# Optimization experiments

Hardware: AMD Instinct MI355X
Metric: run time of the kernel (lower is better)

The kernel has to match this reference:

```python
import jax, jax.numpy as jnp
import numpy as np

B, L, D, H, MLP = 8, 1024, 768, 12, 3072
DH = D // H
EPS = 1e-5


def setup_inputs() -> dict:
    key = jax.random.key(0)
    ks = jax.random.split(key, 8)
    s = 0.02
    return {
        "x": jax.random.normal(ks[0], (B, L, D), dtype=jnp.float32),
        "ln1_g": jnp.ones((D,), jnp.float32),
        "ln1_b": jnp.zeros((D,), jnp.float32),
        "w_qkv": jax.random.normal(ks[1], (3 * D, D), dtype=jnp.float32) * s,
        "w_out": jax.random.normal(ks[2], (D, D), dtype=jnp.float32) * s,
        "b_out": jnp.zeros((D,), jnp.float32),
        "ln2_g": jnp.ones((D,), jnp.float32),
        "ln2_b": jnp.zeros((D,), jnp.float32),
        "w1": jax.random.normal(ks[3], (MLP, D), dtype=jnp.float32) * s,
        "b1": jnp.zeros((MLP,), jnp.float32),
        "w2": jax.random.normal(ks[4], (D, MLP), dtype=jnp.float32) * s,
        "b2": jnp.zeros((D,), jnp.float32),
    }


def _layernorm(x, g, b):
    mu = jnp.mean(x, axis=-1, keepdims=True)
    var = jnp.mean(jnp.square(x - mu), axis=-1, keepdims=True)
    return (x - mu) * jax.lax.rsqrt(var + EPS) * g + b


def reference(x, ln1_g, ln1_b, w_qkv, w_out, b_out, ln2_g, ln2_b, w1, b1, w2, b2):
    # --- self-attention branch ---
    xn = _layernorm(x, ln1_g, ln1_b)                     # [B, L, D]
    qkv = jnp.einsum('bld,ed->ble', xn, w_qkv)           # [B, L, 3D]
    # rearrange 'b l (qkv h d) -> qkv b h l d'
    qkv = qkv.reshape(B, L, 3, H, DH).transpose(2, 0, 3, 1, 4)
    q, k, v = qkv[0], qkv[1], qkv[2]                     # [B, H, L, DH]
    scale = DH ** -0.5
    att = jnp.einsum('bhxd,bhyd->bhxy', q, k) * scale    # [B, H, L, L]
    att = jax.nn.softmax(att, axis=-1)
    o = jnp.einsum('bhxy,bhyd->bhxd', att, v)            # [B, H, L, DH]
    o = o.transpose(0, 2, 1, 3).reshape(B, L, D)         # 'b h l d -> b l (h d)'
    o = jnp.einsum('bld,ed->ble', o, w_out) + b_out
    x = x + o
    # --- MLP branch ---
    xn = _layernorm(x, ln2_g, ln2_b)
    h = jax.nn.gelu(jnp.einsum('bld,md->blm', xn, w1) + b1, approximate=False)
    h = jnp.einsum('blm,dm->bld', h, w2) + b2
    return x + h
```

## Files before the change

kernel.cpp:

```cpp
#include <hip/hip_runtime.h>
#include <hip/hip_bf16.h>
#include <math.h>

#define NB 8
#define NL 1024
#define ND 768
#define NH 12
#define NDH 64
#define NMLP 3072
#define NROWS 8192

typedef __attribute__((ext_vector_type(8))) short short8;
typedef __attribute__((ext_vector_type(8))) __bf16 bf16x8;
typedef __attribute__((ext_vector_type(4))) float f32x4;
typedef __attribute__((ext_vector_type(4))) float float4v;
typedef __attribute__((ext_vector_type(4))) unsigned short ushort4v;

__device__ __forceinline__ unsigned short f2b(float f) {
  unsigned u = __float_as_uint(f);
  unsigned r = (u + 0x7fffu + ((u >> 16) & 1u)) >> 16;
  return (unsigned short)r;
}

__device__ __forceinline__ f32x4 mfma16(short8 a, short8 b, f32x4 c) {
  return __builtin_amdgcn_mfma_f32_16x16x32_bf16(
      __builtin_bit_cast(bf16x8, a), __builtin_bit_cast(bf16x8, b), c, 0, 0, 0);
}

__device__ __forceinline__ void gl_lds16(const void* g, void* l) {
  __builtin_amdgcn_global_load_lds(
      (__attribute__((address_space(1))) void*)g,
      (__attribute__((address_space(3))) void*)l, 16, 0, 0);
}

__global__ __launch_bounds__(256) void cvt_bf16(const float* __restrict__ s,
                                                unsigned short* __restrict__ d,
                                                int n) {
  int i = (blockIdx.x * 256 + threadIdx.x) * 4;
  if (i < n) {
    float4v v = *(const float4v*)(s + i);
    ushort4v o;
    o[0] = f2b(v[0]); o[1] = f2b(v[1]); o[2] = f2b(v[2]); o[3] = f2b(v[3]);
    *(ushort4v*)(d + i) = o;
  }
}

__global__ __launch_bounds__(256) void ln_bf16(const float* __restrict__ x,
                                               const float* __restrict__ g,
                                               const float* __restrict__ b,
                                               unsigned short* __restrict__ out) {
  int row = blockIdx.x, tid = threadIdx.x;
  const float* xr = x + (size_t)row * ND;
  float v0 = xr[tid], v1 = xr[tid + 256], v2 = xr[tid + 512];
  float s = v0 + v1 + v2;
  __shared__ float red[8];
#pragma unroll
  for (int o = 32; o > 0; o >>= 1) s += __shfl_down(s, o);
  int wv = tid >> 6, ln = tid & 63;
  if (ln == 0) red[wv] = s;
  __syncthreads();
  float mu = (red[0] + red[1] + red[2] + red[3]) * (1.0f / 768.0f);
  float d0 = v0 - mu, d1 = v1 - mu, d2 = v2 - mu;
  float q = d0 * d0 + d1 * d1 + d2 * d2;
#pragma unroll
  for (int o = 32; o > 0; o >>= 1) q += __shfl_down(q, o);
  if (ln == 0) red[4 + wv] = q;
  __syncthreads();
  float var = (red[4] + red[5] + red[6] + red[7]) * (1.0f / 768.0f);
  float rs = rsqrtf(var + 1e-5f);
  unsigned short* orow = out + (size_t)row * ND;
  orow[tid]       = f2b(d0 * rs * g[tid]       + b[tid]);
  orow[tid + 256] = f2b(d1 * rs * g[tid + 256] + b[tid + 256]);
  orow[tid + 512] = f2b(d2 * rs * g[tid + 512] + b[tid + 512]);
}

template <int MODE, int BM>
__global__ __launch_bounds__(256) void gemm_bt(
    const unsigned short* __restrict__ A, const unsigned short* __restrict__ W,
    unsigned short* __restrict__ outB, float* __restrict__ outF,
    const float* __restrict__ bias, const float* __restrict__ resid,
    int M, int N, int K, int gx) {
  constexpr int WN = (BM == 128) ? 2 : 4;
  constexpr int NJ = 128 / (WN * 16);
  __shared__ __attribute__((aligned(16))) unsigned short As[2 * BM * 32];
  __shared__ __attribute__((aligned(16))) unsigned short Bs[2 * 128 * 32];

  const int nwg = gridDim.x;
  const int bid = blockIdx.x;
  const int q = nwg >> 3, r = nwg & 7;
  const int xcd = bid & 7, idx = bid >> 3;
  const int swz = (xcd < r ? xcd * (q + 1) : r * (q + 1) + (xcd - r) * q) + idx;
  const int by = swz / gx, bx = swz - by * gx;
  const int m0 = by * BM, n0 = bx * 128;

  const int tid = threadIdx.x;
  const int wave = tid >> 6, lane = tid & 63;
  const int l15 = lane & 15, lhi = lane >> 4;
  const int wm = wave / WN, wn = wave % WN;

  const int sr = tid >> 2, sc8 = (tid & 3) * 8;
  const unsigned short* Ag0 = A + (size_t)(m0 + sr) * K + sc8;
  const unsigned short* Ag1 = Ag0 + (size_t)64 * K;
  const unsigned short* Wg0 = W + (size_t)(n0 + sr) * K + sc8;
  const unsigned short* Wg1 = Wg0 + (size_t)64 * K;

  f32x4 acc[4][NJ];
#pragma unroll
  for (int i = 0; i < 4; i++)
#pragma unroll
    for (int j = 0; j < NJ; j++) acc[i][j] = (f32x4){0.f, 0.f, 0.f, 0.f};

  auto STAGE = [&](int k0v, int buf) {
    unsigned short* Ad = As + buf * (BM * 32) + wave * 512;
    unsigned short* Bd = Bs + buf * 4096 + wave * 512;
    gl_lds16(Ag0 + k0v, Ad);
    if constexpr (BM == 128) gl_lds16(Ag1 + k0v, Ad + 2048);
    gl_lds16(Wg0 + k0v, Bd);
    gl_lds16(Wg1 + k0v, Bd + 2048);
  };

  STAGE(0, 0);

  for (int k0 = 0; k0 < K; k0 += 32) {
    const int cb = (k0 >> 5) & 1;
    if (k0 + 32 < K) {
      STAGE(k0 + 32, cb ^ 1);
      if constexpr (BM == 128)
        asm volatile("s_waitcnt vmcnt(4)" ::: "memory");
      else
        asm volatile("s_waitcnt vmcnt(3)" ::: "memory");
    } else {
      asm volatile("s_waitcnt vmcnt(0)" ::: "memory");
    }
    __builtin_amdgcn_s_barrier();

    const unsigned short* Ac = As + cb * (BM * 32);
    const unsigned short* Bc = Bs + cb * 4096;
    short8 af[4], bf[NJ];
#pragma unroll
    for (int i = 0; i < 4; i++)
      af[i] = *(const short8*)&Ac[(wm * 64 + i * 16 + l15) * 32 + lhi * 8];
#pragma unroll
    for (int j = 0; j < NJ; j++)
      bf[j] = *(const short8*)&Bc[(wn * (NJ * 16) + j * 16 + l15) * 32 + lhi * 8];
#pragma unroll
    for (int i = 0; i < 4; i++)
#pragma unroll
      for (int j = 0; j < NJ; j++) acc[i][j] = mfma16(af[i], bf[j], acc[i][j]);

    __builtin_amdgcn_s_barrier();
  }

#pragma unroll
  for (int i = 0; i < 4; i++) {
    int row = m0 + wm * 64 + i * 16 + lhi * 4;
#pragma unroll
    for (int j = 0; j < NJ; j++) {
      int col = n0 + wn * (NJ * 16) + j * 16 + l15;
#pragma unroll
      for (int r2 = 0; r2 < 4; r2++) {
        float v = acc[i][j][r2];
        size_t idxo = (size_t)(row + r2) * N + col;
        if (MODE == 0) {
          outB[idxo] = f2b(v);
        } else if (MODE == 2) {
          float t = v + bias[col];
          outB[idxo] = f2b(0.5f * t * (1.0f + erff(t * 0.70710678118f)));
        } else {
          outF[idxo] = v + bias[col] + resid[idxo];
        }
      }
    }
  }
}

__global__ __launch_bounds__(256) void vtrans(const unsigned short* __restrict__ qkv,
                                              unsigned short* __restrict__ vT) {
  int bid = blockIdx.x;
  int tt = bid & 15;
  int t2 = bid >> 4;
  int h = t2 % NH, b = t2 / NH;
  __shared__ unsigned short L[64 * 72];
  int t = threadIdx.x;
  int row0 = t >> 3;
  int col8 = (t & 7) * 8;
#pragma unroll
  for (int s = 0; s < 2; s++) {
    int row = row0 + s * 32;
    const unsigned short* src =
        qkv + ((size_t)(b * NL + tt * 64 + row)) * 2304 + 1536 + h * 64 + col8;
    short8 v = *(const short8*)src;
    int wchunk = row >> 3;
#pragma unroll
    for (int j = 0; j < 8; j++) {
      int d = col8 + j;
      int cp = wchunk ^ (d >> 3);
      L[d * 72 + cp * 8 + (row & 7)] = (unsigned short)v[j];
    }
  }
  __syncthreads();
#pragma unroll
  for (int s = 0; s < 2; s++) {
    int d = (t >> 3) + s * 32;
    int rc = t & 7;
    int cp = rc ^ (d >> 3);
    short8 ov = *(const short8*)&L[d * 72 + cp * 8];
    *(short8*)(vT + ((size_t)((b * NH + h) * 64 + d)) * NL + tt * 64 + rc * 8) = ov;
  }
}

__global__ __launch_bounds__(256, 3) void attn_kernel(
    const unsigned short* __restrict__ qkv, const unsigned short* __restrict__ vT,
    unsigned short* __restrict__ o) {
  int bid = blockIdx.x;
  int qt = bid & 7;
  int t = bid >> 3;
  int h = t % NH, b = t / NH;
  const int tid = threadIdx.x;
  const int wave = tid >> 6, lane = tid & 63;
  const int l15 = lane & 15, lhi = lane >> 4;
  const int sw = l15 & 7;
  __shared__ __attribute__((aligned(16))) unsigned short Ks[2 * 64 * 64];
  __shared__ __attribute__((aligned(16))) unsigned short Vs[2 * 64 * 64];
  __shared__ __attribute__((aligned(16))) unsigned short Ps[4 * 16 * 64];

  const unsigned short* qp = qkv + (size_t)(b * NL + qt * 128) * 2304 + h * 64;
  short8 qf[2][2];
#pragma unroll
  for (int i = 0; i < 2; i++)
#pragma unroll
    for (int kk = 0; kk < 2; kk++)
      qf[i][kk] = *(const short8*)(qp + (size_t)(i * 64 + wave * 16 + l15) * 2304 +
                                   kk * 32 + lhi * 8);

  const int srow = tid >> 3, scpos = tid & 7;
  const int sc8 = (scpos ^ (srow & 7)) * 8;
  const unsigned short* ks0 =
      qkv + (size_t)(b * NL + srow) * 2304 + 768 + h * 64 + sc8;
  const unsigned short* vt0 =
      vT + (size_t)((b * NH + h) * 64 + srow) * NL + sc8;
  unsigned short* Pw = Ps + wave * 1024;

  float mrow[2][4];
  f32x4 acc[2][4];
  f32x4 accL[2];
#pragma unroll
  for (int i = 0; i < 2; i++) {
#pragma unroll
    for (int r = 0; r < 4; r++) mrow[i][r] = -1e30f;
    accL[i] = (f32x4){0.f, 0.f, 0.f, 0.f};
#pragma unroll
    for (int nb = 0; nb < 4; nb++) acc[i][nb] = (f32x4){0.f, 0.f, 0.f, 0.f};
  }

  short8 onesf;
#pragma unroll
  for (int j = 0; j < 8; j++) onesf[j] = (short)0x3F80;

#define STAGE(ktile, buf)                                                    \
  {                                                                          \
    const unsigned short* ksrc = ks0 + (size_t)((ktile) * 64) * 2304;        \
    const unsigned short* vsrc = vt0 + (ktile) * 64;                         \
    unsigned short* kb_ = Ks + (buf) * 4096 + wave * 512;                    \
    unsigned short* vb_ = Vs + (buf) * 4096 + wave * 512;                    \
    gl_lds16(ksrc, kb_);                                                     \
    gl_lds16(ksrc + (size_t)32 * 2304, kb_ + 2048);                          \
    gl_lds16(vsrc, vb_);                                                     \
    gl_lds16(vsrc + 32 * NL, vb_ + 2048);                                    \
  }

  STAGE(0, 0);

  for (int kt = 0; kt < 16; kt++) {
    const int cb = kt & 1;
    if (kt + 1 < 16) {
      STAGE(kt + 1, cb ^ 1);
      asm volatile("s_waitcnt vmcnt(4)" ::: "memory");
    } else {
      asm volatile("s_waitcnt vmcnt(0)" ::: "memory");
    }
    __builtin_amdgcn_s_barrier();

    const unsigned short* Kc = Ks + cb * 4096;
    const unsigned short* Vc = Vs + cb * 4096;

    short8 vf[4][2];
#pragma unroll
    for (int nb = 0; nb < 4; nb++)
#pragma unroll
      for (int kk = 0; kk < 2; kk++)
        vf[nb][kk] =
            *(const short8*)&Vc[(nb * 16 + l15) * 64 + ((kk * 4 + lhi) ^ sw) * 8];

#pragma unroll
    for (int i = 0; i < 2; i++) {
      f32x4 sv[4];
#pragma unroll
      for (int kb = 0; kb < 4; kb++) {
        short8 kf0 = *(const short8*)&Kc[(kb * 16 + l15) * 64 + (lhi ^ sw) * 8];
        short8 kf1 = *(const short8*)&Kc[(kb * 16 + l15) * 64 + ((4 + lhi) ^ sw) * 8];
        f32x4 s = mfma16(qf[i][0], kf0, (f32x4){0.f, 0.f, 0.f, 0.f});
        sv[kb] = mfma16(qf[i][1], kf1, s);
      }
      float xmax[4];
#pragma unroll
      for (int r = 0; r < 4; r++) {
        float x = fmaxf(fmaxf(sv[0][r], sv[1][r]), fmaxf(sv[2][r], sv[3][r]));
#pragma unroll
        for (int m = 1; m < 16; m <<= 1) x = fmaxf(x, __shfl_xor(x, m));
        xmax[r] = x;
      }
      bool ok = (xmax[0] <= mrow[i][0] + 64.f) & (xmax[1] <= mrow[i][1] + 64.f) &
                (xmax[2] <= mrow[i][2] + 64.f) & (xmax[3] <= mrow[i][3] + 64.f);
      if (!__all(ok)) {
#pragma unroll
        for (int r = 0; r < 4; r++) {
          float mnew = fmaxf(mrow[i][r], xmax[r]);
          float corr = __expf((mrow[i][r] - mnew) * 0.125f);
          mrow[i][r] = mnew;
#pragma unroll
          for (int nb = 0; nb < 4; nb++) acc[i][nb][r] *= corr;
          accL[i][r] *= corr;
        }
      }
      float mm[4];
#pragma unroll
      for (int r = 0; r < 4; r++) mm[r] = -mrow[i][r] * 0.125f;
#pragma unroll
      for (int kb = 0; kb < 4; kb++) {
        int ch = kb * 2 + (l15 >> 3);
#pragma unroll
        for (int r = 0; r < 4; r++) {
          int row = lhi * 4 + r;
          float p = __expf(fmaf(sv[kb][r], 0.125f, mm[r]));
          unsigned short pu =
              (unsigned short)((__float_as_uint(p) + 0x8000u) >> 16);
          Pw[row * 64 + ((ch ^ (row & 7)) << 3) + sw] = pu;
        }
      }
      short8 pf0 = *(const short8*)&Pw[l15 * 64 + (lhi ^ sw) * 8];
      short8 pf1 = *(const short8*)&Pw[l15 * 64 + ((4 + lhi) ^ sw) * 8];
#pragma unroll
      for (int nb = 0; nb < 4; nb++) {
        acc[i][nb] = mfma16(pf0, vf[nb][0], acc[i][nb]);
        acc[i][nb] = mfma16(pf1, vf[nb][1], acc[i][nb]);
      }
      accL[i] = mfma16(pf0, onesf, accL[i]);
      accL[i] = mfma16(pf1, onesf, accL[i]);
    }
    __builtin_amdgcn_s_barrier();
  }
#undef STAGE

#pragma unroll
  for (int i = 0; i < 2; i++) {
    float inv[4];
#pragma unroll
    for (int r = 0; r < 4; r++) inv[r] = 1.0f / accL[i][r];
    size_t obase =
        (size_t)(b * NL + qt * 128 + i * 64 + wave * 16 + lhi * 4) * ND + h * 64;
#pragma unroll
    for (int nb = 0; nb < 4; nb++)
#pragma unroll
      for (int r = 0; r < 4; r++)
        o[obase + (size_t)r * ND + nb * 16 + l15] = f2b(acc[i][nb][r] * inv[r]);
  }
}

extern "C" void kernel_launch(void* const* d_in, const int* in_sizes, int n_in,
                              void* d_out, int out_size, void* d_ws, size_t ws_size,
                              hipStream_t stream) {
  const float* x     = (const float*)d_in[0];
  const float* ln1_g = (const float*)d_in[1];
  const float* ln1_b = (const float*)d_in[2];
  const float* w_qkv = (const float*)d_in[3];
  const float* w_out = (const float*)d_in[4];
  const float* b_out = (const float*)d_in[5];
  const float* ln2_g = (const float*)d_in[6];
  const float* ln2_b = (const float*)d_in[7];
  const float* w1    = (const float*)d_in[8];
  const float* b1    = (const float*)d_in[9];
  const float* w2    = (const float*)d_in[10];
  const float* b2    = (const float*)d_in[11];
  float* out = (float*)d_out;

  char* p = (char*)d_ws;
  unsigned short* wqkv_b = (unsigned short*)p; p += (size_t)2304 * 768 * 2;
  unsigned short* wout_b = (unsigned short*)p; p += (size_t)768 * 768 * 2;
  unsigned short* w1_b   = (unsigned short*)p; p += (size_t)3072 * 768 * 2;
  unsigned short* w2_b   = (unsigned short*)p; p += (size_t)768 * 3072 * 2;
  unsigned short* xn     = (unsigned short*)p; p += (size_t)NROWS * ND * 2;
  unsigned short* qkvb   = (unsigned short*)p; p += (size_t)NROWS * NMLP * 2;
  float* x1 = (float*)p;  p += (size_t)NROWS * ND * 4;
  unsigned short* vTb = (unsigned short*)x1;

  cvt_bf16<<<(2304 * 768 / 4 + 255) / 256, 256, 0, stream>>>(w_qkv, wqkv_b, 2304 * 768);
  cvt_bf16<<<(768 * 768 / 4 + 255) / 256, 256, 0, stream>>>(w_out, wout_b, 768 * 768);
  cvt_bf16<<<(3072 * 768 / 4 + 255) / 256, 256, 0, stream>>>(w1, w1_b, 3072 * 768);
  cvt_bf16<<<(768 * 3072 / 4 + 255) / 256, 256, 0, stream>>>(w2, w2_b, 768 * 3072);

  ln_bf16<<<NROWS, 256, 0, stream>>>(x, ln1_g, ln1_b, xn);
  gemm_bt<0, 128><<<1152, 256, 0, stream>>>(
      xn, wqkv_b, qkvb, nullptr, nullptr, nullptr, NROWS, 2304, 768, 18);
  vtrans<<<NB * NH * (NL / 64), 256, 0, stream>>>(qkvb, vTb);
  attn_kernel<<<NB * NH * (NL / 128), 256, 0, stream>>>(qkvb, vTb, xn);
  gemm_bt<1, 64><<<768, 256, 0, stream>>>(
      xn, wout_b, nullptr, x1, b_out, x, NROWS, 768, 768, 6);
  ln_bf16<<<NROWS, 256, 0, stream>>>(x1, ln2_g, ln2_b, xn);
  gemm_bt<2, 128><<<1536, 256, 0, stream>>>(
      xn, w1_b, qkvb, nullptr, b1, nullptr, NROWS, 3072, 768, 24);
  gemm_bt<3, 64><<<768, 256, 0, stream>>>(
      qkvb, w2_b, nullptr, out, b2, x1, NROWS, 768, 3072, 6);
}
```

Before: 304.7 us.

## Triple-buffer GEMM K loop, fuse weight casts, approximate GELU with tanh form

The GEMM main loop goes from a two-stage to a three-stage LDS ring, so loads for tile t+2 are in flight while tile t is computed, with adjusted vmcnt waits and an explicit lgkmcnt wait before the barrier. The four weight-conversion launches become one kernel that maps each index range to its source tensor and writes into one contiguous workspace. The exact erf GELU in the MLP GEMM epilogue is replaced by the tanh approximation written as x*sigmoid(z) with fast exp and divide. This changes numerics away from the exact GELU the reference requires, and the extra buffer increases LDS use per block, which may lower occupancy.

```diff
diff --git a/kernel.cpp b/kernel.cpp
--- a/kernel.cpp
+++ b/kernel.cpp
@@ -33,16 +33,22 @@
       (__attribute__((address_space(3))) void*)l, 16, 0, 0);
 }
 
-__global__ __launch_bounds__(256) void cvt_bf16(const float* __restrict__ s,
-                                                unsigned short* __restrict__ d,
-                                                int n) {
+__global__ __launch_bounds__(256) void cvt_all(const float* __restrict__ s0,
+                                               const float* __restrict__ s1,
+                                               const float* __restrict__ s2,
+                                               const float* __restrict__ s3,
+                                               unsigned short* __restrict__ d) {
   int i = (blockIdx.x * 256 + threadIdx.x) * 4;
-  if (i < n) {
-    float4v v = *(const float4v*)(s + i);
-    ushort4v o;
-    o[0] = f2b(v[0]); o[1] = f2b(v[1]); o[2] = f2b(v[2]); o[3] = f2b(v[3]);
-    *(ushort4v*)(d + i) = o;
-  }
+  const float* s;
+  int off;
+  if (i < 1769472) { s = s0; off = i; }
+  else if (i < 2359296) { s = s1; off = i - 1769472; }
+  else if (i < 4718592) { s = s2; off = i - 2359296; }
+  else { s = s3; off = i - 4718592; }
+  float4v v = *(const float4v*)(s + off);
+  ushort4v o;
+  o[0] = f2b(v[0]); o[1] = f2b(v[1]); o[2] = f2b(v[2]); o[3] = f2b(v[3]);
+  *(ushort4v*)(d + i) = o;
 }
 
 __global__ __launch_bounds__(256) void ln_bf16(const float* __restrict__ x,
@@ -82,8 +88,9 @@
     int M, int N, int K, int gx) {
   constexpr int WN = (BM == 128) ? 2 : 4;
   constexpr int NJ = 128 / (WN * 16);
-  __shared__ __attribute__((aligned(16))) unsigned short As[2 * BM * 32];
-  __shared__ __attribute__((aligned(16))) unsigned short Bs[2 * 128 * 32];
+  constexpr int LDSA = BM * 32;
+  __shared__ __attribute__((aligned(16))) unsigned short As[3 * LDSA];
+  __shared__ __attribute__((aligned(16))) unsigned short Bs[3 * 4096];
 
   const int nwg = gridDim.x;
   const int bid = blockIdx.x;
@@ -110,21 +117,28 @@
 #pragma unroll
     for (int j = 0; j < NJ; j++) acc[i][j] = (f32x4){0.f, 0.f, 0.f, 0.f};
 
-  auto STAGE = [&](int k0v, int buf) {
-    unsigned short* Ad = As + buf * (BM * 32) + wave * 512;
+  auto STAGE = [&](int kelem, int buf) {
+    unsigned short* Ad = As + buf * LDSA + wave * 512;
     unsigned short* Bd = Bs + buf * 4096 + wave * 512;
-    gl_lds16(Ag0 + k0v, Ad);
-    if constexpr (BM == 128) gl_lds16(Ag1 + k0v, Ad + 2048);
-    gl_lds16(Wg0 + k0v, Bd);
-    gl_lds16(Wg1 + k0v, Bd + 2048);
+    gl_lds16(Ag0 + kelem, Ad);
+    if constexpr (BM == 128) gl_lds16(Ag1 + kelem, Ad + 2048);
+    gl_lds16(Wg0 + kelem, Bd);
+    gl_lds16(Wg1 + kelem, Bd + 2048);
   };
 
+  const int NT = K >> 5;
   STAGE(0, 0);
-
-  for (int k0 = 0; k0 < K; k0 += 32) {
-    const int cb = (k0 >> 5) & 1;
-    if (k0 + 32 < K) {
-      STAGE(k0 + 32, cb ^ 1);
+  STAGE(32, 1);
+
+  int cb = 0, nbuf = 2;
+  for (int t = 0; t < NT; ++t) {
+    if (t + 2 < NT) {
+      STAGE((t + 2) * 32, nbuf);
+      if constexpr (BM == 128)
+        asm volatile("s_waitcnt vmcnt(8)" ::: "memory");
+      else
+        asm volatile("s_waitcnt vmcnt(6)" ::: "memory");
+    } else if (t + 2 == NT) {
       if constexpr (BM == 128)
         asm volatile("s_waitcnt vmcnt(4)" ::: "memory");
       else
@@ -134,7 +148,7 @@
     }
     __builtin_amdgcn_s_barrier();
 
-    const unsigned short* Ac = As + cb * (BM * 32);
+    const unsigned short* Ac = As + cb * LDSA;
     const unsigned short* Bc = Bs + cb * 4096;
     short8 af[4], bf[NJ];
 #pragma unroll
@@ -148,7 +162,10 @@
 #pragma unroll
       for (int j = 0; j < NJ; j++) acc[i][j] = mfma16(af[i], bf[j], acc[i][j]);
 
+    asm volatile("s_waitcnt lgkmcnt(0)" ::: "memory");
     __builtin_amdgcn_s_barrier();
+    cb = (cb == 2) ? 0 : cb + 1;
+    nbuf = (nbuf == 2) ? 0 : nbuf + 1;
   }
 
 #pragma unroll
@@ -164,8 +181,10 @@
         if (MODE == 0) {
           outB[idxo] = f2b(v);
         } else if (MODE == 2) {
-          float t = v + bias[col];
-          outB[idxo] = f2b(0.5f * t * (1.0f + erff(t * 0.70710678118f)));
+          float t2 = v + bias[col];
+          float z = 1.5957691f * t2 * (1.0f + 0.044715f * t2 * t2);
+          float e = __expf(-z);
+          outB[idxo] = f2b(__fdividef(t2, 1.0f + e));
         } else {
           outF[idxo] = v + bias[col] + resid[idxo];
         }
@@ -394,10 +413,7 @@
   float* x1 = (float*)p;  p += (size_t)NROWS * ND * 4;
   unsigned short* vTb = (unsigned short*)x1;
 
-  cvt_bf16<<<(2304 * 768 / 4 + 255) / 256, 256, 0, stream>>>(w_qkv, wqkv_b, 2304 * 768);
-  cvt_bf16<<<(768 * 768 / 4 + 255) / 256, 256, 0, stream>>>(w_out, wout_b, 768 * 768);
-  cvt_bf16<<<(3072 * 768 / 4 + 255) / 256, 256, 0, stream>>>(w1, w1_b, 3072 * 768);
-  cvt_bf16<<<(768 * 3072 / 4 + 255) / 256, 256, 0, stream>>>(w2, w2_b, 768 * 3072);
+  cvt_all<<<7077888 / 4 / 256, 256, 0, stream>>>(w_qkv, w_out, w1, w2, wqkv_b);
 
   ln_bf16<<<NROWS, 256, 0, stream>>>(x, ln1_g, ln1_b, xn);
   gemm_bt<0, 128><<<1152, 256, 0, stream>>>(
```

After: 296.0 us. 2.8% less time.
